# Performance work log

Measured on AMD Instinct MI355X. Metric: run time of the kernel, lower is better.

## Reference

```python
import jax, jax.numpy as jnp
import numpy as np

DEPTH, HEADS, DIM_HEAD = 6, 12, 64
DIM, MLP, FEAT = 768, 3072, 1000
B, N = 32, 196
EPS = 1e-5


def layernorm(x, g, b):
    m = jnp.mean(x, axis=-1, keepdims=True)
    v = jnp.var(x, axis=-1, keepdims=True)
    return (x - m) * jax.lax.rsqrt(v + EPS) * g + b


def setup_inputs() -> dict:
    key = jax.random.key(0)
    ks = jax.random.split(key, 8)
    s = 0.02
    return {
        "x": jax.random.normal(ks[0], (B, N, DIM), jnp.float32),
        "cls_token": jax.random.normal(ks[1], (1, 1, DIM), jnp.float32),
        "ln1_g": jnp.ones((DEPTH, DIM), jnp.float32),
        "ln1_b": jnp.zeros((DEPTH, DIM), jnp.float32),
        "w_qkv": jax.random.normal(ks[2], (DEPTH, DIM, 3 * HEADS * DIM_HEAD), jnp.float32) * s,
        "reattn_w": jax.random.normal(ks[3], (DEPTH, HEADS, HEADS), jnp.float32),
        "reattn_g": jnp.ones((DEPTH, HEADS), jnp.float32),
        "reattn_b": jnp.zeros((DEPTH, HEADS), jnp.float32),
        "w_out": jax.random.normal(ks[4], (DEPTH, HEADS * DIM_HEAD, DIM), jnp.float32) * s,
        "b_out": jnp.zeros((DEPTH, DIM), jnp.float32),
        "ln2_g": jnp.ones((DEPTH, DIM), jnp.float32),
        "ln2_b": jnp.zeros((DEPTH, DIM), jnp.float32),
        "w1": jax.random.normal(ks[5], (DEPTH, DIM, MLP), jnp.float32) * s,
        "b1": jnp.zeros((DEPTH, MLP), jnp.float32),
        "w2": jax.random.normal(ks[6], (DEPTH, MLP, DIM), jnp.float32) * s,
        "b2": jnp.zeros((DEPTH, DIM), jnp.float32),
        "lnf_g": jnp.ones((DIM,), jnp.float32),
        "lnf_b": jnp.zeros((DIM,), jnp.float32),
        "w_head": jax.random.normal(ks[7], (DIM, FEAT), jnp.float32) * s,
        "b_head": jnp.zeros((FEAT,), jnp.float32),
    }


def _forward(x, cls_token, ln1_g, ln1_b, w_qkv, reattn_w, reattn_g, reattn_b,
             w_out, b_out, ln2_g, ln2_b, w1, b1, w2, b2, lnf_g, lnf_b, w_head, b_head):
    b = x.shape[0]
    cls = jnp.broadcast_to(cls_token, (b, 1, DIM))
    x = jnp.concatenate([cls, x], axis=1)  # (B, N+1, DIM)
    n = x.shape[1]
    scale = DIM_HEAD ** -0.5
    for l in range(DEPTH):
        h = layernorm(x, ln1_g[l], ln1_b[l])
        qkv = h @ w_qkv[l]                       # (B, n, 3*H*Dh)
        qkv = qkv.reshape(b, n, 3, HEADS, DIM_HEAD)
        q, k, v = (qkv[:, :, i].transpose(0, 2, 1, 3) for i in range(3))  # b h n d
        dots = jnp.einsum('bhid,bhjd->bhij', q, k) * scale
        attn = jax.nn.softmax(dots, axis=-1)
        attn = jnp.einsum('bhij,hg->bgij', attn, reattn_w[l])
        # per-head LayerNorm: normalize over head axis (axis=1)
        m = jnp.mean(attn, axis=1, keepdims=True)
        var = jnp.var(attn, axis=1, keepdims=True)
        attn = (attn - m) * jax.lax.rsqrt(var + EPS)
        attn = attn * reattn_g[l][None, :, None, None] + reattn_b[l][None, :, None, None]
        out = jnp.einsum('bhij,bhjd->bhid', attn, v)
        out = out.transpose(0, 2, 1, 3).reshape(b, n, HEADS * DIM_HEAD)
        x = x + out @ w_out[l] + b_out[l]
        h = layernorm(x, ln2_g[l], ln2_b[l])
        h = jax.nn.gelu(h @ w1[l] + b1[l], approximate=False)
        x = x + h @ w2[l] + b2[l]
    pooled = x[:, 0]  # cls pool
    return layernorm(pooled, lnf_g, lnf_b) @ w_head + b_head


def reference(x, cls_token, ln1_g, ln1_b, w_qkv, reattn_w, reattn_g, reattn_b,
              w_out, b_out, ln2_g, ln2_b, w1, b1, w2, b2, lnf_g, lnf_b, w_head, b_head):
    return _forward(x, cls_token, ln1_g, ln1_b, w_qkv, reattn_w, reattn_g, reattn_b,
                    w_out, b_out, ln2_g, ln2_b, w1, b1, w2, b2, lnf_g, lnf_b, w_head, b_head)
```

## Files before the change

### kernel.cpp

```cpp
#include <hip/hip_runtime.h>
#include <cstdint>

typedef __bf16 bf16_t;
typedef __bf16 bf16x8 __attribute__((ext_vector_type(8)));
typedef float  f32x4  __attribute__((ext_vector_type(4)));
typedef unsigned int u32;

#define DEPTH 6
#define HEADS 12
#define DH    64
#define DIM   768
#define MLPD  3072
#define FEAT  1000
#define BATCH 32
#define SEQ   197
#define NP    224
#define TOK   (BATCH*SEQ)

__device__ __forceinline__ f32x4 zero4() {
    f32x4 z; z[0] = 0.f; z[1] = 0.f; z[2] = 0.f; z[3] = 0.f; return z;
}

__device__ __forceinline__ f32x4 mfma16(bf16x8 a, bf16x8 b, f32x4 c) {
    return __builtin_amdgcn_mfma_f32_16x16x32_bf16(a, b, c, 0, 0, 0);
}

typedef const __attribute__((address_space(1))) u32* gas_ptr;
typedef __attribute__((address_space(3))) u32*       las_ptr;
__device__ __forceinline__ void gload16(const bf16_t* g, bf16_t* l) {
    __builtin_amdgcn_global_load_lds((gas_ptr)g, (las_ptr)l, 16, 0, 0);
}

__device__ __forceinline__ int xcd_logical(int L, int nblk) {
    int q = nblk >> 3, r = nblk & 7, xcd = L & 7;
    return (xcd < r ? xcd * (q + 1) : r * (q + 1) + (xcd - r) * q) + (L >> 3);
}

__global__ __launch_bounds__(256) void concat_k(const float* __restrict__ x,
                                                const float* __restrict__ cls,
                                                float* __restrict__ xbuf) {
    int idx = blockIdx.x * 256 + threadIdx.x;
    int col = idx % DIM;
    int row = idx / DIM;
    int b = row / SEQ, p = row % SEQ;
    xbuf[idx] = (p == 0) ? cls[col] : x[(b * 196 + p - 1) * DIM + col];
}

__global__ __launch_bounds__(256) void tcvt_k(const float* __restrict__ W,
                                              bf16_t* __restrict__ Wt,
                                              int K, int N) {
    __shared__ float t[32][33];
    int n0 = blockIdx.x * 32, k0 = blockIdx.y * 32;
    int c = threadIdx.x & 31, r = threadIdx.x >> 5;
#pragma unroll
    for (int i = 0; i < 4; i++) {
        int k = k0 + r + i * 8, n = n0 + c;
        t[r + i * 8][c] = (n < N) ? W[k * N + n] : 0.f;
    }
    __syncthreads();
#pragma unroll
    for (int i = 0; i < 4; i++) {
        int n = n0 + r + i * 8, k = k0 + c;
        if (n < N) Wt[n * K + k] = (bf16_t)t[c][r + i * 8];
    }
}

__global__ __launch_bounds__(256) void ln_k(const float* __restrict__ x, long row_stride,
                                            const float* __restrict__ g,
                                            const float* __restrict__ b,
                                            bf16_t* __restrict__ out) {
    int row = blockIdx.x;
    const float* xr = x + (long)row * row_stride;
    int t = threadIdx.x;
    float v0 = xr[t], v1 = xr[t + 256], v2 = xr[t + 512];
    float s  = v0 + v1 + v2;
    float sq = v0 * v0 + v1 * v1 + v2 * v2;
#pragma unroll
    for (int o = 1; o < 64; o <<= 1) { s += __shfl_xor(s, o); sq += __shfl_xor(sq, o); }
    __shared__ float ss[4], sqs[4];
    int w = t >> 6;
    if ((t & 63) == 0) { ss[w] = s; sqs[w] = sq; }
    __syncthreads();
    s  = ss[0] + ss[1] + ss[2] + ss[3];
    sq = sqs[0] + sqs[1] + sqs[2] + sqs[3];
    float m  = s * (1.f / 768.f);
    float rs = rsqrtf(sq * (1.f / 768.f) - m * m + 1e-5f);
    bf16_t* orow = out + (long)row * DIM;
    orow[t]       = (bf16_t)((v0 - m) * rs * g[t]       + b[t]);
    orow[t + 256] = (bf16_t)((v1 - m) * rs * g[t + 256] + b[t + 256]);
    orow[t + 512] = (bf16_t)((v2 - m) * rs * g[t + 512] + b[t + 512]);
}

template <int MODE>
__global__ __launch_bounds__(256, 3) void gemm_k(const bf16_t* __restrict__ A,
                                                 const bf16_t* __restrict__ Bt,
                                                 const float* __restrict__ bias,
                                                 float* __restrict__ Cf,
                                                 bf16_t* __restrict__ Cb,
                                                 int M, int N, int K, int nN) {
    __shared__ bf16_t sA[3][128 * 32];
    __shared__ bf16_t sB[3][128 * 32];
    bf16_t* sa = &sA[0][0];
    bf16_t* sb = &sB[0][0];
    int tid = threadIdx.x;
    int g = xcd_logical(blockIdx.x, gridDim.x);
    int bm = (g / nN) * 128, bn = (g % nN) * 128;
    int wave = tid >> 6, lane = tid & 63;
    int wm = (wave >> 1) * 64, wn = (wave & 1) * 64;
    int la = lane & 15, lb = lane >> 4;

    int tq = tid >> 2;
    int scol = ((tid & 3) ^ ((tid >> 3) & 3)) * 8;
    int a0 = bm + tq;      if (a0 > M - 1) a0 = M - 1;
    int a1 = bm + 64 + tq; if (a1 > M - 1) a1 = M - 1;
    int b0 = bn + tq, b1 = bn + 64 + tq;
    int wslot = wave * 512;

    int lbx = (lb ^ ((la >> 1) & 3)) << 3;

    f32x4 acc[4][4];
#pragma unroll
    for (int m = 0; m < 4; m++)
#pragma unroll
        for (int n = 0; n < 4; n++) acc[m][n] = zero4();

    int NT = K >> 5;

    auto stage = [&](int buf, int kt) {
        int k0 = kt << 5;
        gload16(A  + (long)a0 * K + k0 + scol, sa + buf * 4096 + wslot);
        gload16(A  + (long)a1 * K + k0 + scol, sa + buf * 4096 + 2048 + wslot);
        gload16(Bt + (long)b0 * K + k0 + scol, sb + buf * 4096 + wslot);
        gload16(Bt + (long)b1 * K + k0 + scol, sb + buf * 4096 + 2048 + wslot);
    };

    stage(0, 0);
    stage(1, 1);

    for (int t = 0; t < NT; t++) {
        if (t < NT - 1) asm volatile("s_waitcnt vmcnt(4)" ::: "memory");
        else            asm volatile("s_waitcnt vmcnt(0)" ::: "memory");
        __builtin_amdgcn_s_barrier();
        asm volatile("" ::: "memory");

        if (t + 2 < NT) stage((t + 2) % 3, t + 2);

        const bf16_t* cA = sa + (t % 3) * 4096;
        const bf16_t* cB = sb + (t % 3) * 4096;
        bf16x8 av[4], bv[4];
#pragma unroll
        for (int mf = 0; mf < 4; mf++)
            av[mf] = *(const bf16x8*)(cA + (wm + mf * 16 + la) * 32 + lbx);
#pragma unroll
        for (int nf = 0; nf < 4; nf++)
            bv[nf] = *(const bf16x8*)(cB + (wn + nf * 16 + la) * 32 + lbx);
        __builtin_amdgcn_s_setprio(1);
#pragma unroll
        for (int mf = 0; mf < 4; mf++)
#pragma unroll
            for (int nf = 0; nf < 4; nf++)
                acc[mf][nf] = mfma16(av[mf], bv[nf], acc[mf][nf]);
        __builtin_amdgcn_s_setprio(0);
    }

#pragma unroll
    for (int mf = 0; mf < 4; mf++) {
#pragma unroll
        for (int nf = 0; nf < 4; nf++) {
            int ib = bm + wm + mf * 16 + lb * 4;
            int jb = bn + wn + nf * 16 + la;
            float bvv = (MODE == 0) ? 0.f : bias[jb];
#pragma unroll
            for (int rr = 0; rr < 4; rr++) {
                int i = ib + rr;
                if (i >= M) continue;
                float v = acc[mf][nf][rr];
                if (MODE == 0) {
                    Cb[(long)i * N + jb] = (bf16_t)v;
                } else if (MODE == 1) {
                    Cf[(long)i * N + jb] += v + bvv;
                } else {
                    float u = v + bvv;
                    Cb[(long)i * N + jb] = (bf16_t)(0.5f * u * (1.f + erff(u * 0.70710678118f)));
                }
            }
        }
    }
}

__global__ __launch_bounds__(256) void gemm_h(const bf16_t* __restrict__ A,
                                              const bf16_t* __restrict__ Bt,
                                              const float* __restrict__ bias,
                                              float* __restrict__ Cf,
                                              int M, int N, int K) {
    __shared__ bf16_t sA[2][128][32];
    __shared__ bf16_t sB[2][128][32];
    int tid = threadIdx.x;
    int bm = blockIdx.x * 128, bn = blockIdx.y * 128;
    int wave = tid >> 6, lane = tid & 63;
    int wm = (wave >> 1) * 64, wn = (wave & 1) * 64;
    int la = lane & 15, lb = lane >> 4;
    int rowA[2], rowB[2], colE[2];
#pragma unroll
    for (int q = 0; q < 2; q++) {
        int li = (wave * 2 + q) * 64 + lane;
        int row = li >> 2;
        colE[q] = (li & 3) * 8;
        int ar = bm + row; if (ar > M - 1) ar = M - 1;
        int br = bn + row; if (br > N - 1) br = N - 1;
        rowA[q] = ar; rowB[q] = br;
    }
    f32x4 acc[4][4];
#pragma unroll
    for (int m = 0; m < 4; m++)
#pragma unroll
        for (int n = 0; n < 4; n++) acc[m][n] = zero4();
    int nt = K >> 5;
#pragma unroll
    for (int q = 0; q < 2; q++) {
        gload16(A  + (long)rowA[q] * K + colE[q], &sA[0][0][0] + (wave * 2 + q) * 512);
        gload16(Bt + (long)rowB[q] * K + colE[q], &sB[0][0][0] + (wave * 2 + q) * 512);
    }
    __syncthreads();
    for (int t = 0; t < nt; t++) {
        int cur = t & 1;
        if (t + 1 < nt) {
            int k0 = (t + 1) << 5;
#pragma unroll
            for (int q = 0; q < 2; q++) {
                gload16(A  + (long)rowA[q] * K + k0 + colE[q], &sA[cur ^ 1][0][0] + (wave * 2 + q) * 512);
                gload16(Bt + (long)rowB[q] * K + k0 + colE[q], &sB[cur ^ 1][0][0] + (wave * 2 + q) * 512);
            }
        }
        bf16x8 af[4], bfr[4];
#pragma unroll
        for (int m = 0; m < 4; m++) af[m]  = *(const bf16x8*)&sA[cur][wm + m * 16 + la][lb * 8];
#pragma unroll
        for (int n = 0; n < 4; n++) bfr[n] = *(const bf16x8*)&sB[cur][wn + n * 16 + la][lb * 8];
#pragma unroll
        for (int m = 0; m < 4; m++)
#pragma unroll
            for (int n = 0; n < 4; n++)
                acc[m][n] = mfma16(af[m], bfr[n], acc[m][n]);
        __syncthreads();
    }
#pragma unroll
    for (int m = 0; m < 4; m++) {
#pragma unroll
        for (int n = 0; n < 4; n++) {
            int ib = bm + wm + m * 16 + lb * 4;
            int jb = bn + wn + n * 16 + la;
            if (jb >= N) continue;
            float bv = bias[jb];
#pragma unroll
            for (int r = 0; r < 4; r++) {
                int i = ib + r;
                if (i >= M) continue;
                Cf[(long)i * N + jb] = acc[m][n][r] + bv;
            }
        }
    }
}

__global__ __launch_bounds__(256) void qk_k(const bf16_t* __restrict__ qkv,
                                            float* __restrict__ dots) {
    int bh = blockIdx.z;
    int b = bh / HEADS, h = bh % HEADS;
    int i0 = blockIdx.x * 64, j0 = blockIdx.y * 64;
    __shared__ bf16_t sQ[64][32], sK[64][32];
    int tid = threadIdx.x, wave = tid >> 6, lane = tid & 63;
    int wm = (wave >> 1) * 32, wn = (wave & 1) * 32;
    int la = lane & 15, lb = lane >> 4;
    f32x4 acc[2][2];
#pragma unroll
    for (int m = 0; m < 2; m++)
#pragma unroll
        for (int n = 0; n < 2; n++) acc[m][n] = zero4();

    int row = tid >> 2, col = (tid & 3) * 8;
    int qi = i0 + row; if (qi > SEQ - 1) qi = SEQ - 1;
    int kj = j0 + row; if (kj > SEQ - 1) kj = SEQ - 1;
    const bf16_t* qsrc = qkv + (((b * SEQ + qi) * 3 + 0) * HEADS + h) * DH + col;
    const bf16_t* ksrc = qkv + (((b * SEQ + kj) * 3 + 1) * HEADS + h) * DH + col;

#pragma unroll
    for (int d0 = 0; d0 < 64; d0 += 32) {
        *(bf16x8*)&sQ[row][col] = *(const bf16x8*)(qsrc + d0);
        *(bf16x8*)&sK[row][col] = *(const bf16x8*)(ksrc + d0);
        __syncthreads();
        bf16x8 af[2], bfr[2];
#pragma unroll
        for (int m = 0; m < 2; m++) af[m]  = *(const bf16x8*)&sQ[wm + m * 16 + la][lb * 8];
#pragma unroll
        for (int n = 0; n < 2; n++) bfr[n] = *(const bf16x8*)&sK[wn + n * 16 + la][lb * 8];
#pragma unroll
        for (int m = 0; m < 2; m++)
#pragma unroll
            for (int n = 0; n < 2; n++)
                acc[m][n] = mfma16(af[m], bfr[n], acc[m][n]);
        __syncthreads();
    }
#pragma unroll
    for (int m = 0; m < 2; m++)
#pragma unroll
        for (int n = 0; n < 2; n++)
#pragma unroll
            for (int r = 0; r < 4; r++) {
                int i = i0 + wm + m * 16 + lb * 4 + r;
                int j = j0 + wn + n * 16 + la;
                if (i < SEQ && j < SEQ)
                    dots[((long)bh * SEQ + i) * NP + j] = acc[m][n][r] * 0.125f;
            }
}

__global__ __launch_bounds__(256) void smre_k(const float* __restrict__ dots,
                                              const float* __restrict__ W,
                                              const float* __restrict__ gg,
                                              const float* __restrict__ bb,
                                              bf16_t* __restrict__ attn2) {
    __shared__ float sm[HEADS][NP];
    __shared__ float sW[HEADS * HEADS];
    __shared__ float sg[HEADS], sb[HEADS];
    int tid = threadIdx.x;
    if (tid < HEADS * HEADS) sW[tid] = W[tid];
    if (tid < HEADS) { sg[tid] = gg[tid]; sb[tid] = bb[tid]; }
    int bi = blockIdx.x;
    int b = bi / SEQ, i = bi % SEQ;
    int wave = tid >> 6, lane = tid & 63;

    for (int h = wave; h < HEADS; h += 4) {
        const float* p = dots + ((long)(b * HEADS + h) * SEQ + i) * NP;
        float v[4], e[4];
#pragma unroll
        for (int q = 0; q < 4; q++) { int j = lane + 64 * q; v[q] = (j < SEQ) ? p[j] : -3.0e38f; }
        float mx = fmaxf(fmaxf(v[0], v[1]), fmaxf(v[2], v[3]));
#pragma unroll
        for (int o = 1; o < 64; o <<= 1) mx = fmaxf(mx, __shfl_xor(mx, o));
        float s = 0.f;
#pragma unroll
        for (int q = 0; q < 4; q++) {
            int j = lane + 64 * q;
            e[q] = (j < SEQ) ? __expf(v[q] - mx) : 0.f;
            s += e[q];
        }
#pragma unroll
        for (int o = 1; o < 64; o <<= 1) s += __shfl_xor(s, o);
        float inv = 1.f / s;
#pragma unroll
        for (int q = 0; q < 4; q++) { int j = lane + 64 * q; if (j < NP) sm[h][j] = e[q] * inv; }
    }
    __syncthreads();

    int j = tid;
    if (j >= NP) return;
    bool valid = j < SEQ;
    float vals[HEADS];
#pragma unroll
    for (int h = 0; h < HEADS; h++) vals[h] = valid ? sm[h][j] : 0.f;
    float mix[HEADS];
    float s = 0.f, sq = 0.f;
#pragma unroll
    for (int g = 0; g < HEADS; g++) {
        float a = 0.f;
#pragma unroll
        for (int h = 0; h < HEADS; h++) a += vals[h] * sW[h * HEADS + g];
        mix[g] = a; s += a; sq += a * a;
    }
    float m  = s * (1.f / 12.f);
    float rs = rsqrtf(sq * (1.f / 12.f) - m * m + 1e-5f);
    long base = ((long)(b * HEADS) * SEQ + i) * NP + j;
    const long hs = (long)SEQ * NP;
#pragma unroll
    for (int g = 0; g < HEADS; g++) {
        float o = valid ? ((mix[g] - m) * rs * sg[g] + sb[g]) : 0.f;
        attn2[base + g * hs] = (bf16_t)o;
    }
}

__global__ __launch_bounds__(256) void pv_k(const bf16_t* __restrict__ attn2,
                                            const bf16_t* __restrict__ qkv,
                                            bf16_t* __restrict__ aout) {
    int bh = blockIdx.y;
    int b = bh / HEADS, h = bh % HEADS;
    int i0 = blockIdx.x * 64;
    __shared__ bf16_t sP[64][32];
    __shared__ bf16_t sVt[64][32];
    int tid = threadIdx.x, wave = tid >> 6, lane = tid & 63;
    int wm = (wave >> 1) * 32, wn = (wave & 1) * 32;
    int la = lane & 15, lb = lane >> 4;
    f32x4 acc[2][2];
#pragma unroll
    for (int m = 0; m < 2; m++)
#pragma unroll
        for (int n = 0; n < 2; n++) acc[m][n] = zero4();

    int prow = tid >> 2, pcol = (tid & 3) * 8;
    int pi = i0 + prow; if (pi > SEQ - 1) pi = SEQ - 1;
    const bf16_t* psrc = attn2 + ((long)bh * SEQ + pi) * NP + pcol;
    int jl = tid >> 3, dblk = (tid & 7) * 8;
    int jlx = jl ^ ((tid & 3) << 3);

    for (int j0 = 0; j0 < NP; j0 += 32) {
        *(bf16x8*)&sP[prow][pcol] = *(const bf16x8*)(psrc + j0);
        int jg = j0 + jl;
        bf16x8 vv;
#pragma unroll
        for (int e = 0; e < 8; e++) vv[e] = (bf16_t)0.f;
        if (jg < SEQ)
            vv = *(const bf16x8*)(qkv + (((b * SEQ + jg) * 3 + 2) * HEADS + h) * DH + dblk);
#pragma unroll
        for (int e = 0; e < 8; e++) sVt[dblk + e][jlx] = vv[e];
        __syncthreads();
        bf16x8 af[2], bfr[2];
#pragma unroll
        for (int m = 0; m < 2; m++) af[m] = *(const bf16x8*)&sP[wm + m * 16 + la][lb * 8];
#pragma unroll
        for (int n = 0; n < 2; n++) {
            int rowd = wn + n * 16 + la;
            int colj = (lb * 8) ^ (((rowd >> 3) & 3) << 3);
            bfr[n] = *(const bf16x8*)&sVt[rowd][colj];
        }
#pragma unroll
        for (int m = 0; m < 2; m++)
#pragma unroll
            for (int n = 0; n < 2; n++)
                acc[m][n] = mfma16(af[m], bfr[n], acc[m][n]);
        __syncthreads();
    }
#pragma unroll
    for (int m = 0; m < 2; m++)
#pragma unroll
        for (int n = 0; n < 2; n++)
#pragma unroll
            for (int r = 0; r < 4; r++) {
                int i = i0 + wm + m * 16 + lb * 4 + r;
                int d = wn + n * 16 + la;
                if (i < SEQ)
                    aout[((long)b * SEQ + i) * DIM + h * DH + d] = (bf16_t)acc[m][n][r];
            }
}

extern "C" void kernel_launch(void* const* d_in, const int* in_sizes, int n_in,
                              void* d_out, int out_size, void* d_ws, size_t ws_size,
                              hipStream_t stream) {
    const float* x        = (const float*)d_in[0];
    const float* cls      = (const float*)d_in[1];
    const float* ln1_g    = (const float*)d_in[2];
    const float* ln1_b    = (const float*)d_in[3];
    const float* w_qkv    = (const float*)d_in[4];
    const float* reattn_w = (const float*)d_in[5];
    const float* reattn_g = (const float*)d_in[6];
    const float* reattn_b = (const float*)d_in[7];
    const float* w_out    = (const float*)d_in[8];
    const float* b_out    = (const float*)d_in[9];
    const float* ln2_g    = (const float*)d_in[10];
    const float* ln2_b    = (const float*)d_in[11];
    const float* w1       = (const float*)d_in[12];
    const float* b1       = (const float*)d_in[13];
    const float* w2       = (const float*)d_in[14];
    const float* b2       = (const float*)d_in[15];
    const float* lnf_g    = (const float*)d_in[16];
    const float* lnf_b    = (const float*)d_in[17];
    const float* w_head   = (const float*)d_in[18];
    const float* b_head   = (const float*)d_in[19];
    float* out = (float*)d_out;

    char* p = (char*)d_ws;
    auto alloc = [&](size_t bytes) -> char* {
        char* r = p;
        p += (bytes + 255) & ~(size_t)255;
        return r;
    };
    bf16_t* wt      = (bf16_t*)alloc(2ULL * MLPD * DIM);
    bf16_t* wt_head = (bf16_t*)alloc(2ULL * FEAT * DIM);
    float*  xbuf    = (float*)alloc(4ULL * TOK * DIM);
    bf16_t* h_ln    = (bf16_t*)alloc(2ULL * TOK * DIM);
    bf16_t* qkv     = (bf16_t*)alloc(2ULL * TOK * 3 * DIM);
    float*  dots    = (float*)alloc(4ULL * BATCH * HEADS * SEQ * NP);
    bf16_t* h_mid   = (bf16_t*)dots;
    bf16_t* attn2   = (bf16_t*)alloc(2ULL * BATCH * HEADS * SEQ * NP);
    bf16_t* aout    = (bf16_t*)alloc(2ULL * TOK * DIM);

    dim3 B256(256);
    const int NM = (TOK + 127) / 128;
    concat_k<<<(TOK * DIM) / 256, B256, 0, stream>>>(x, cls, xbuf);
    tcvt_k<<<dim3((FEAT + 31) / 32, DIM / 32), B256, 0, stream>>>(w_head, wt_head, DIM, FEAT);

    for (int l = 0; l < DEPTH; l++) {
        ln_k<<<TOK, B256, 0, stream>>>(xbuf, DIM, ln1_g + l * DIM, ln1_b + l * DIM, h_ln);
        tcvt_k<<<dim3(2304 / 32, DIM / 32), B256, 0, stream>>>(w_qkv + (long)l * DIM * 2304, wt, DIM, 2304);
        gemm_k<0><<<NM * 18, B256, 0, stream>>>(h_ln, wt, nullptr, nullptr, qkv, TOK, 2304, DIM, 18);
        qk_k<<<dim3(4, 4, BATCH * HEADS), B256, 0, stream>>>(qkv, dots);
        smre_k<<<TOK, B256, 0, stream>>>(
            dots, reattn_w + l * HEADS * HEADS, reattn_g + l * HEADS, reattn_b + l * HEADS, attn2);
        pv_k<<<dim3(4, BATCH * HEADS), B256, 0, stream>>>(attn2, qkv, aout);
        tcvt_k<<<dim3(DIM / 32, DIM / 32), B256, 0, stream>>>(w_out + (long)l * DIM * DIM, wt, DIM, DIM);
        gemm_k<1><<<NM * 6, B256, 0, stream>>>(aout, wt, b_out + l * DIM, xbuf, nullptr, TOK, DIM, DIM, 6);
        ln_k<<<TOK, B256, 0, stream>>>(xbuf, DIM, ln2_g + l * DIM, ln2_b + l * DIM, h_ln);
        tcvt_k<<<dim3(MLPD / 32, DIM / 32), B256, 0, stream>>>(w1 + (long)l * DIM * MLPD, wt, DIM, MLPD);
        gemm_k<2><<<NM * 24, B256, 0, stream>>>(h_ln, wt, b1 + l * MLPD, nullptr, h_mid, TOK, MLPD, DIM, 24);
        tcvt_k<<<dim3(DIM / 32, MLPD / 32), B256, 0, stream>>>(w2 + (long)l * MLPD * DIM, wt, MLPD, DIM);
        gemm_k<1><<<NM * 6, B256, 0, stream>>>(h_mid, wt, b2 + l * DIM, xbuf, nullptr, TOK, DIM, MLPD, 6);
    }

    ln_k<<<BATCH, B256, 0, stream>>>(xbuf, (long)SEQ * DIM, lnf_g, lnf_b, h_ln);
    gemm_h<<<dim3(1, 8), B256, 0, stream>>>(h_ln, wt_head, b_head, out, BATCH, FEAT, DIM);
}
```

Measured before the change: 2.068 ms.

## Split-K the MLP down-projection and widen GEMM k-tiles to 64 with double buffering

Retiles the bf16 GEMM to 64-wide K steps with two shared-memory buffers and an 8-way XOR swizzle, lowering occupancy bound to 2 blocks per CU. Adds a split-K mode that writes fp32 partials for the w2 GEMM over two K halves, followed by a reduction kernel that adds partials, bias and residual. Aims to fill more CUs on the long-K, narrow-N GEMM and cut barrier count per K. Costs an extra partial-sum write/read pass and reuses the attention buffer (spilling into the adjacent buffer) as scratch.

After: 2.015 ms. -2.6%, faster.

```diff
diff --git a/kernel.cpp b/kernel.cpp
--- a/kernel.cpp
+++ b/kernel.cpp
@@ -92,31 +92,33 @@
 }
 
 template <int MODE>
-__global__ __launch_bounds__(256, 3) void gemm_k(const bf16_t* __restrict__ A,
+__global__ __launch_bounds__(256, 2) void gemm_k(const bf16_t* __restrict__ A,
                                                  const bf16_t* __restrict__ Bt,
                                                  const float* __restrict__ bias,
                                                  float* __restrict__ Cf,
                                                  bf16_t* __restrict__ Cb,
-                                                 int M, int N, int K, int nN) {
-    __shared__ bf16_t sA[3][128 * 32];
-    __shared__ bf16_t sB[3][128 * 32];
-    bf16_t* sa = &sA[0][0];
-    bf16_t* sb = &sB[0][0];
+                                                 int M, int N, int Kstride, int Klen,
+                                                 int nN, int nblk) {
+    __shared__ bf16_t sA[2][128 * 64];
+    __shared__ bf16_t sB[2][128 * 64];
     int tid = threadIdx.x;
-    int g = xcd_logical(blockIdx.x, gridDim.x);
+    int kc = blockIdx.x / nblk;
+    int g  = xcd_logical(blockIdx.x % nblk, nblk);
     int bm = (g / nN) * 128, bn = (g % nN) * 128;
+    long koff = (long)kc * Klen;
     int wave = tid >> 6, lane = tid & 63;
     int wm = (wave >> 1) * 64, wn = (wave & 1) * 64;
     int la = lane & 15, lb = lane >> 4;
 
-    int tq = tid >> 2;
-    int scol = ((tid & 3) ^ ((tid >> 3) & 3)) * 8;
-    int a0 = bm + tq;      if (a0 > M - 1) a0 = M - 1;
-    int a1 = bm + 64 + tq; if (a1 > M - 1) a1 = M - 1;
-    int b0 = bn + tq, b1 = bn + 64 + tq;
-    int wslot = wave * 512;
-
-    int lbx = (lb ^ ((la >> 1) & 3)) << 3;
+    int srow = tid >> 3;
+    int scol = ((tid & 7) ^ (srow & 7)) * 8;
+    int rA[4], rB[4];
+#pragma unroll
+    for (int i = 0; i < 4; i++) {
+        int r = bm + i * 32 + srow; rA[i] = (r < M) ? r : M - 1;
+        rB[i] = bn + i * 32 + srow;
+    }
+    int wbase = wave * 512;
 
     f32x4 acc[4][4];
 #pragma unroll
@@ -124,52 +126,58 @@
 #pragma unroll
         for (int n = 0; n < 4; n++) acc[m][n] = zero4();
 
-    int NT = K >> 5;
+    const int NT = Klen >> 6;
+    int swz = la & 7;
 
     auto stage = [&](int buf, int kt) {
-        int k0 = kt << 5;
-        gload16(A  + (long)a0 * K + k0 + scol, sa + buf * 4096 + wslot);
-        gload16(A  + (long)a1 * K + k0 + scol, sa + buf * 4096 + 2048 + wslot);
-        gload16(Bt + (long)b0 * K + k0 + scol, sb + buf * 4096 + wslot);
-        gload16(Bt + (long)b1 * K + k0 + scol, sb + buf * 4096 + 2048 + wslot);
+        long k0 = koff + ((long)kt << 6);
+#pragma unroll
+        for (int i = 0; i < 4; i++)
+            gload16(A + (long)rA[i] * Kstride + k0 + scol, &sA[buf][i * 2048 + wbase]);
+#pragma unroll
+        for (int i = 0; i < 4; i++)
+            gload16(Bt + (long)rB[i] * Kstride + k0 + scol, &sB[buf][i * 2048 + wbase]);
     };
 
     stage(0, 0);
-    stage(1, 1);
 
     for (int t = 0; t < NT; t++) {
-        if (t < NT - 1) asm volatile("s_waitcnt vmcnt(4)" ::: "memory");
-        else            asm volatile("s_waitcnt vmcnt(0)" ::: "memory");
+        int cur = t & 1;
+        asm volatile("s_waitcnt vmcnt(0)" ::: "memory");
         __builtin_amdgcn_s_barrier();
         asm volatile("" ::: "memory");
-
-        if (t + 2 < NT) stage((t + 2) % 3, t + 2);
-
-        const bf16_t* cA = sa + (t % 3) * 4096;
-        const bf16_t* cB = sb + (t % 3) * 4096;
-        bf16x8 av[4], bv[4];
-#pragma unroll
-        for (int mf = 0; mf < 4; mf++)
-            av[mf] = *(const bf16x8*)(cA + (wm + mf * 16 + la) * 32 + lbx);
-#pragma unroll
-        for (int nf = 0; nf < 4; nf++)
-            bv[nf] = *(const bf16x8*)(cB + (wn + nf * 16 + la) * 32 + lbx);
-        __builtin_amdgcn_s_setprio(1);
-#pragma unroll
-        for (int mf = 0; mf < 4; mf++)
+        if (t + 1 < NT) stage(cur ^ 1, t + 1);
+
+        const bf16_t* cA = &sA[cur][0];
+        const bf16_t* cB = &sB[cur][0];
+#pragma unroll
+        for (int ks = 0; ks < 2; ks++) {
+            bf16x8 aR[4], bR[4];
+            int gr = ((ks * 4 + lb) ^ swz) << 3;
+#pragma unroll
+            for (int mf = 0; mf < 4; mf++)
+                aR[mf] = *(const bf16x8*)(cA + (wm + mf * 16 + la) * 64 + gr);
 #pragma unroll
             for (int nf = 0; nf < 4; nf++)
-                acc[mf][nf] = mfma16(av[mf], bv[nf], acc[mf][nf]);
-        __builtin_amdgcn_s_setprio(0);
-    }
-
+                bR[nf] = *(const bf16x8*)(cB + (wn + nf * 16 + la) * 64 + gr);
+            __builtin_amdgcn_s_setprio(1);
+#pragma unroll
+            for (int mf = 0; mf < 4; mf++)
+#pragma unroll
+                for (int nf = 0; nf < 4; nf++)
+                    acc[mf][nf] = mfma16(aR[mf], bR[nf], acc[mf][nf]);
+            __builtin_amdgcn_s_setprio(0);
+        }
+    }
+
+    long kout = (long)kc * M * (long)N;
 #pragma unroll
     for (int mf = 0; mf < 4; mf++) {
 #pragma unroll
         for (int nf = 0; nf < 4; nf++) {
             int ib = bm + wm + mf * 16 + lb * 4;
             int jb = bn + wn + nf * 16 + la;
-            float bvv = (MODE == 0) ? 0.f : bias[jb];
+            float bvv = (MODE == 1 || MODE == 2) ? bias[jb] : 0.f;
 #pragma unroll
             for (int rr = 0; rr < 4; rr++) {
                 int i = ib + rr;
@@ -179,12 +187,24 @@
                     Cb[(long)i * N + jb] = (bf16_t)v;
                 } else if (MODE == 1) {
                     Cf[(long)i * N + jb] += v + bvv;
-                } else {
+                } else if (MODE == 2) {
                     float u = v + bvv;
                     Cb[(long)i * N + jb] = (bf16_t)(0.5f * u * (1.f + erff(u * 0.70710678118f)));
+                } else {
+                    Cf[kout + (long)i * N + jb] = v;
                 }
             }
         }
+    }
+}
+
+__global__ __launch_bounds__(256) void redk_k(float* __restrict__ xbuf,
+                                              const float* __restrict__ part,
+                                              const float* __restrict__ bias) {
+    const long total = (long)TOK * DIM;
+    for (long idx = blockIdx.x * 256 + threadIdx.x; idx < total; idx += (long)gridDim.x * 256) {
+        int col = (int)(idx % DIM);
+        xbuf[idx] += part[idx] + part[idx + total] + bias[col];
     }
 }
 
@@ -480,6 +500,7 @@
     bf16_t* h_mid   = (bf16_t*)dots;
     bf16_t* attn2   = (bf16_t*)alloc(2ULL * BATCH * HEADS * SEQ * NP);
     bf16_t* aout    = (bf16_t*)alloc(2ULL * TOK * DIM);
+    float*  part    = (float*)attn2;
 
     dim3 B256(256);
     const int NM = (TOK + 127) / 128;
@@ -489,18 +510,23 @@
     for (int l = 0; l < DEPTH; l++) {
         ln_k<<<TOK, B256, 0, stream>>>(xbuf, DIM, ln1_g + l * DIM, ln1_b + l * DIM, h_ln);
         tcvt_k<<<dim3(2304 / 32, DIM / 32), B256, 0, stream>>>(w_qkv + (long)l * DIM * 2304, wt, DIM, 2304);
-        gemm_k<0><<<NM * 18, B256, 0, stream>>>(h_ln, wt, nullptr, nullptr, qkv, TOK, 2304, DIM, 18);
+        gemm_k<0><<<NM * 18, B256, 0, stream>>>(h_ln, wt, nullptr, nullptr, qkv,
+                                                TOK, 2304, DIM, DIM, 18, NM * 18);
         qk_k<<<dim3(4, 4, BATCH * HEADS), B256, 0, stream>>>(qkv, dots);
         smre_k<<<TOK, B256, 0, stream>>>(
             dots, reattn_w + l * HEADS * HEADS, reattn_g + l * HEADS, reattn_b + l * HEADS, attn2);
         pv_k<<<dim3(4, BATCH * HEADS), B256, 0, stream>>>(attn2, qkv, aout);
         tcvt_k<<<dim3(DIM / 32, DIM / 32), B256, 0, stream>>>(w_out + (long)l * DIM * DIM, wt, DIM, DIM);
-        gemm_k<1><<<NM * 6, B256, 0, stream>>>(aout, wt, b_out + l * DIM, xbuf, nullptr, TOK, DIM, DIM, 6);
+        gemm_k<1><<<NM * 6, B256, 0, stream>>>(aout, wt, b_out + l * DIM, xbuf, nullptr,
+                                               TOK, DIM, DIM, DIM, 6, NM * 6);
         ln_k<<<TOK, B256, 0, stream>>>(xbuf, DIM, ln2_g + l * DIM, ln2_b + l * DIM, h_ln);
         tcvt_k<<<dim3(MLPD / 32, DIM / 32), B256, 0, stream>>>(w1 + (long)l * DIM * MLPD, wt, DIM, MLPD);
-        gemm_k<2><<<NM * 24, B256, 0, stream>>>(h_ln, wt, b1 + l * MLPD, nullptr, h_mid, TOK, MLPD, DIM, 24);
+        gemm_k<2><<<NM * 24, B256, 0, stream>>>(h_ln, wt, b1 + l * MLPD, nullptr, h_mid,
+                                                TOK, MLPD, DIM, DIM, 24, NM * 24);
         tcvt_k<<<dim3(DIM / 32, MLPD / 32), B256, 0, stream>>>(w2 + (long)l * MLPD * DIM, wt, MLPD, DIM);
-        gemm_k<1><<<NM * 6, B256, 0, stream>>>(h_mid, wt, b2 + l * DIM, xbuf, nullptr, TOK, DIM, MLPD, 6);
+        gemm_k<3><<<NM * 6 * 2, B256, 0, stream>>>(h_mid, wt, nullptr, part, nullptr,
+                                                   TOK, DIM, MLPD, MLPD / 2, 6, NM * 6);
+        redk_k<<<2048, B256, 0, stream>>>(xbuf, part, b2 + l * DIM);
     }
 
     ln_k<<<BATCH, B256, 0, stream>>>(xbuf, (long)SEQ * DIM, lnf_g, lnf_b, h_ln);
```
